# Kernel tuning notes

Measured on AMD Instinct MI355X. Metric: run time of the kernel, lower is better.

The kernel has to match this reference:

```python
import jax, jax.numpy as jnp
import numpy as np

EPS = 1e-6
BETA = 0.25
COMMIT_W = 1.0


def setup_inputs() -> dict:
    key = jax.random.key(0)
    k1, k2, k3 = jax.random.split(key, 3)
    b, c, h, w = 8, 256, 32, 32
    n_e, e_dim = 16384, 256
    z = jax.random.normal(k1, (b, c, h, w), jnp.float32)
    # frozen_codebook = randn(n_e, e_dim) * e_dim**-0.5
    codebook = jax.random.normal(k2, (n_e, e_dim), jnp.float32) * (e_dim ** -0.5)
    # nn.Linear(e_dim, in_channels, bias=False) weight: (in_channels, e_dim)
    W = jax.random.normal(k3, (c, e_dim), jnp.float32) * (e_dim ** -0.5)
    return {"z": z, "codebook": codebook, "W": W}


def _rotate_to(src, tgt):
    # Rotation trick (Fifty et al.): rotate src onto tgt direction with a
    # detached Householder-style transform; gradient flows through src only.
    # src, tgt: (n, d)
    norm_src = jnp.linalg.norm(src, axis=-1, keepdims=True)
    norm_tgt = jnp.linalg.norm(tgt, axis=-1, keepdims=True)
    u = src / (norm_src + EPS)
    q = tgt / (norm_tgt + EPS)
    uq = u + q
    w_ = jax.lax.stop_gradient(uq / (jnp.linalg.norm(uq, axis=-1, keepdims=True) + EPS))
    u_d = jax.lax.stop_gradient(u)
    q_d = jax.lax.stop_gradient(q)
    rot = (src
           - 2.0 * jnp.sum(src * w_, axis=-1, keepdims=True) * w_
           + 2.0 * jnp.sum(src * u_d, axis=-1, keepdims=True) * q_d)
    return rot * jax.lax.stop_gradient(norm_tgt / (norm_src + EPS))


def reference(z, codebook, W):
    b, c, h, w = z.shape
    # b c h w -> (b*h*w, c)
    z_flat = jnp.transpose(z, (0, 2, 3, 1)).reshape(-1, c)
    # implicit codebook: frozen codes through linear projection
    emb = codebook @ W.T  # (n_e, c)
    # squared L2 distances (no grad needed for argmin)
    d = (jnp.sum(z_flat ** 2, axis=1, keepdims=True)
         + jnp.sum(emb ** 2, axis=1)
         - 2.0 * (z_flat @ emb.T))  # (n_tok, n_e)
    indices = jnp.argmin(d, axis=1)  # (n_tok,)
    z_q_flat = emb[indices]  # gather quantized vectors
    loss = COMMIT_W * (jnp.mean((jax.lax.stop_gradient(z_flat) - z_q_flat) ** 2)
                       + BETA * jnp.mean((z_flat - jax.lax.stop_gradient(z_q_flat)) ** 2))
    z_q_flat = _rotate_to(z_flat, z_q_flat)
    z_q = jnp.transpose(z_q_flat.reshape(b, h, w, c), (0, 3, 1, 2))
    return z_q, loss, indices
```

## Files before the change

### kernel.cpp

```cpp
#include <hip/hip_runtime.h>
#include <math.h>

#define EPSV 1e-6f
#define NTOK 8192
#define NE   16384
#define DIM  256

using short8 = __attribute__((ext_vector_type(8))) short;
using f32x4v = __attribute__((ext_vector_type(4))) float;

__device__ __forceinline__ unsigned short f2bf(float v) {
    unsigned int u = __float_as_uint(v);
    u += 0x7fffu + ((u >> 16) & 1u);
    return (unsigned short)(u >> 16);
}
__device__ __forceinline__ float bf2f(unsigned short h) {
    return __uint_as_float(((unsigned int)h) << 16);
}

__device__ __forceinline__ void gload_lds16(const void* g, void* s) {
    __builtin_amdgcn_global_load_lds(
        (const __attribute__((address_space(1))) void*)g,
        (__attribute__((address_space(3))) void*)s, 16, 0, 0);
}

__device__ __forceinline__ void split8(const float4 a, const float4 b,
                                       short8& h, short8& l) {
    float f[8] = {a.x, a.y, a.z, a.w, b.x, b.y, b.z, b.w};
#pragma unroll
    for (int j = 0; j < 8; ++j) {
        unsigned short hh = f2bf(f[j]);
        h[j] = (short)hh;
        l[j] = (short)f2bf(f[j] - bf2f(hh));
    }
}

__global__ __launch_bounds__(256) void f1_pre(
    const float* __restrict__ zin, float* __restrict__ z_flat,
    unsigned short* __restrict__ zh, unsigned short* __restrict__ zl,
    float* __restrict__ sz, const float* __restrict__ Wm,
    unsigned short* __restrict__ wh, unsigned short* __restrict__ wl) {
    const int bid = blockIdx.x;
    const int tid = threadIdx.x;
    if (bid >= 128) {
        const int i = ((bid - 128) * 256 + tid) * 4;
        const float4 v = *(const float4*)(Wm + i);
        float f[4] = {v.x, v.y, v.z, v.w};
#pragma unroll
        for (int j = 0; j < 4; ++j) {
            unsigned short h = f2bf(f[j]);
            wh[i + j] = h;
            wl[i + j] = f2bf(f[j] - bf2f(h));
        }
        return;
    }
    __shared__ float tile[64][65];
    const int yx0 = (bid & 15) * 64, b = bid >> 4;
    const int sub = tid >> 6, ln = tid & 63;
    double dacc[16];
#pragma unroll
    for (int j = 0; j < 16; ++j) dacc[j] = 0.0;

    for (int cc = 0; cc < 4; ++cc) {
        const int c0 = cc * 64;
        __syncthreads();
#pragma unroll
        for (int j = 0; j < 16; ++j) {
            int cl = j * 4 + sub;
            tile[cl][ln] = zin[((size_t)(b * 256 + c0 + cl) << 10) + yx0 + ln];
        }
        __syncthreads();
#pragma unroll
        for (int j = 0; j < 16; ++j) {
            int tl = j * 4 + sub;
            float v = tile[ln][tl];
            size_t o = (size_t)(b * 1024 + yx0 + tl) * 256 + c0 + ln;
            z_flat[o] = v;
            unsigned short h = f2bf(v);
            zh[o] = h;
            zl[o] = f2bf(v - bf2f(h));
            dacc[j] += (double)v * v;
        }
    }
#pragma unroll
    for (int j = 0; j < 16; ++j) {
        double s = dacc[j];
#pragma unroll
        for (int m = 1; m < 64; m <<= 1) s += __shfl_xor(s, m);
        if (ln == 0) sz[b * 1024 + yx0 + j * 4 + sub] = (float)s;
    }
}

__global__ __launch_bounds__(256, 2) void k0c_emb(
    const float* __restrict__ cb, const unsigned short* __restrict__ wh,
    const unsigned short* __restrict__ wl, float* __restrict__ emb,
    unsigned short* __restrict__ eh, unsigned short* __restrict__ el,
    float* __restrict__ se0, float* __restrict__ se1) {
    __shared__ char smemC[65536];
    const int tid = threadIdx.x;
    const int w = tid >> 6, lane = tid & 63;
    const int quad = lane >> 4, lr = lane & 15;
    const int wr = w & 1, wc = w >> 1;
    const int n0 = blockIdx.x * 128, c0 = blockIdx.y * 128;

    f32x4v acc[4][4];
#pragma unroll
    for (int mt = 0; mt < 4; ++mt)
#pragma unroll
        for (int nt = 0; nt < 4; ++nt)
            acc[mt][nt] = (f32x4v){0.f, 0.f, 0.f, 0.f};

    for (int kc = 0; kc < 4; ++kc) {
        __syncthreads();
#pragma unroll
        for (int i = 0; i < 16; ++i) {
            int s = i * 4 + w;
            int u = s * 64 + lane;
            const void* g;
            if (s < 32) {
                int kg = u >> 7, row = u & 127;
                g = cb + (size_t)(n0 + row) * 256 + kc * 64 + kg * 4;
            } else if (s < 48) {
                int u1 = u - 2048;
                int kg = u1 >> 7, row = u1 & 127;
                g = wh + (size_t)(c0 + row) * 256 + kc * 64 + kg * 8;
            } else {
                int u2 = u - 3072;
                int kg = u2 >> 7, row = u2 & 127;
                g = wl + (size_t)(c0 + row) * 256 + kc * 64 + kg * 8;
            }
            gload_lds16(g, smemC + ((size_t)u << 4));
        }
        __syncthreads();
#pragma unroll
        for (int ks = 0; ks < 2; ++ks) {
            short8 Ah[4], Al[4], Bh[4], Bl[4];
#pragma unroll
            for (int mt = 0; mt < 4; ++mt) {
                int m = wr * 64 + mt * 16 + lr;
                int kg2 = ks * 8 + quad * 2;
                float4 f0 = *(const float4*)(smemC + (((size_t)kg2 * 128 + m) << 4));
                float4 f1 = *(const float4*)(smemC + ((((size_t)kg2 + 1) * 128 + m) << 4));
                split8(f0, f1, Ah[mt], Al[mt]);
            }
#pragma unroll
            for (int nt = 0; nt < 4; ++nt) {
                int n = wc * 64 + nt * 16 + lr;
                int ku = (ks * 4 + quad) * 128 + n;
                Bh[nt] = *(const short8*)(smemC + (((size_t)2048 + ku) << 4));
                Bl[nt] = *(const short8*)(smemC + (((size_t)3072 + ku) << 4));
            }
#pragma unroll
            for (int mt = 0; mt < 4; ++mt)
#pragma unroll
                for (int nt = 0; nt < 4; ++nt) {
                    f32x4v a = acc[mt][nt];
                    a = __builtin_amdgcn_mfma_f32_16x16x32_bf16(Ah[mt], Bh[nt], a, 0, 0, 0);
                    a = __builtin_amdgcn_mfma_f32_16x16x32_bf16(Ah[mt], Bl[nt], a, 0, 0, 0);
                    a = __builtin_amdgcn_mfma_f32_16x16x32_bf16(Al[mt], Bh[nt], a, 0, 0, 0);
                    a = __builtin_amdgcn_mfma_f32_16x16x32_bf16(Al[mt], Bl[nt], a, 0, 0, 0);
                    acc[mt][nt] = a;
                }
        }
    }
#pragma unroll
    for (int mt = 0; mt < 4; ++mt)
#pragma unroll
        for (int rr = 0; rr < 4; ++rr) {
            int row = n0 + wr * 64 + mt * 16 + quad * 4 + rr;
#pragma unroll
            for (int nt = 0; nt < 4; ++nt) {
                int col = c0 + wc * 64 + nt * 16 + lr;
                size_t o = (size_t)row * 256 + col;
                float v = acc[mt][nt][rr];
                emb[o] = v;
                unsigned short h = f2bf(v);
                eh[o] = h;
                el[o] = f2bf(v - bf2f(h));
            }
        }
    __syncthreads();
    float* sblk = (float*)smemC;
#pragma unroll
    for (int mt = 0; mt < 4; ++mt)
#pragma unroll
        for (int rr = 0; rr < 4; ++rr) {
            float s = 0.f;
#pragma unroll
            for (int nt = 0; nt < 4; ++nt) {
                float v = acc[mt][nt][rr];
                s = fmaf(v, v, s);
            }
#pragma unroll
            for (int st = 1; st < 16; st <<= 1) s += __shfl_xor(s, st);
            if (lr == 0)
                sblk[wc * 128 + wr * 64 + mt * 16 + quad * 4 + rr] = s;
        }
    __syncthreads();
    if (tid < 128) {
        float* sep = (blockIdx.y == 0) ? se0 : se1;
        sep[n0 + tid] = sblk[tid] + sblk[128 + tid];
    }
}

__global__ __launch_bounds__(256, 2) void k1_dist_argmin(
    const unsigned short* __restrict__ zh, const unsigned short* __restrict__ zl,
    const unsigned short* __restrict__ eh, const unsigned short* __restrict__ el,
    const float* __restrict__ sz, const float* __restrict__ se0,
    const float* __restrict__ se1, float* __restrict__ pval,
    int* __restrict__ pidx) {
    __shared__ short8 smem[2][2048];
    const int tid = threadIdx.x;
    const int w = tid >> 6, lane = tid & 63;
    const int quad = lane >> 4, lr = lane & 15;
    const int tokBase = blockIdx.x * 128;
    const int rowBase = tokBase + w * 32;
    const int slab = blockIdx.y;
    const int slabBase = slab * 2048;

    short8 Ah[2][8], Al[2][8];
#pragma unroll
    for (int mt = 0; mt < 2; ++mt)
#pragma unroll
        for (int ks = 0; ks < 8; ++ks) {
            size_t o = (size_t)(rowBase + mt * 16 + lr) * 256 + ks * 32 + quad * 8;
            Ah[mt][ks] = *(const short8*)(zh + o);
            Al[mt][ks] = *(const short8*)(zl + o);
        }

    float szr[2][4];
#pragma unroll
    for (int mt = 0; mt < 2; ++mt)
#pragma unroll
        for (int rr = 0; rr < 4; ++rr)
            szr[mt][rr] = sz[rowBase + mt * 16 + quad * 4 + rr];

    float minv[2][4];
    int mini[2][4];
#pragma unroll
    for (int mt = 0; mt < 2; ++mt)
#pragma unroll
        for (int rr = 0; rr < 4; ++rr) {
            minv[mt][rr] = INFINITY;
            mini[mt][rr] = 0;
        }

    auto stage = [&](int buf, int ch) {
        const int colBase = slabBase + ch * 32;
#pragma unroll
        for (int i = 0; i < 8; ++i) {
            int u = i * 256 + tid;
            int fmt = u >> 10;
            int u1 = u & 1023;
            int col = u1 >> 5, kgs = u1 & 31;
            int kg = kgs ^ col;
            const unsigned short* g =
                (fmt ? el : eh) + (size_t)(colBase + col) * 256 + kg * 8;
            gload_lds16(g, (char*)&smem[0][0] + buf * 32768 +
                               (((size_t)i * 256 + w * 64) << 4));
        }
    };

    stage(0, 0);
    __syncthreads();

    for (int ch = 0; ch < 64; ++ch) {
        const int cur = ch & 1;
        if (ch + 1 < 64) stage(cur ^ 1, ch + 1);

        const int colg0 = slabBase + ch * 32 + lr;
        const int colg1 = colg0 + 16;
        const float sec0 = se0[colg0] + se1[colg0];
        const float sec1 = se0[colg1] + se1[colg1];

        f32x4v acc[2][2];
#pragma unroll
        for (int mt = 0; mt < 2; ++mt)
#pragma unroll
            for (int nt = 0; nt < 2; ++nt)
                acc[mt][nt] = (f32x4v){0.f, 0.f, 0.f, 0.f};

#pragma unroll
        for (int ks = 0; ks < 8; ++ks) {
            short8 Bh[2], Bl[2];
#pragma unroll
            for (int nt = 0; nt < 2; ++nt) {
                int col = nt * 16 + lr;
                int kgs = (ks * 4 + quad) ^ col;
                Bh[nt] = smem[cur][col * 32 + kgs];
                Bl[nt] = smem[cur][1024 + col * 32 + kgs];
            }
#pragma unroll
            for (int mt = 0; mt < 2; ++mt)
#pragma unroll
                for (int nt = 0; nt < 2; ++nt) {
                    f32x4v a = acc[mt][nt];
                    a = __builtin_amdgcn_mfma_f32_16x16x32_bf16(Ah[mt][ks], Bh[nt], a, 0, 0, 0);
                    a = __builtin_amdgcn_mfma_f32_16x16x32_bf16(Ah[mt][ks], Bl[nt], a, 0, 0, 0);
                    a = __builtin_amdgcn_mfma_f32_16x16x32_bf16(Al[mt][ks], Bh[nt], a, 0, 0, 0);
                    acc[mt][nt] = a;
                }
        }

        const int colBase = slabBase + ch * 32;
#pragma unroll
        for (int nt = 0; nt < 2; ++nt) {
            const int colg = colBase + nt * 16 + lr;
            const float sec = nt ? sec1 : sec0;
#pragma unroll
            for (int mt = 0; mt < 2; ++mt)
#pragma unroll
                for (int rr = 0; rr < 4; ++rr) {
                    float szse = __fadd_rn(szr[mt][rr], sec);
                    float d = fmaf(-2.0f, acc[mt][nt][rr], szse);
                    if (d < minv[mt][rr]) {
                        minv[mt][rr] = d;
                        mini[mt][rr] = colg;
                    }
                }
        }
        __syncthreads();
    }

#pragma unroll
    for (int st = 1; st < 16; st <<= 1) {
#pragma unroll
        for (int mt = 0; mt < 2; ++mt)
#pragma unroll
            for (int rr = 0; rr < 4; ++rr) {
                float ov = __shfl_xor(minv[mt][rr], st);
                int oi = __shfl_xor(mini[mt][rr], st);
                if (ov < minv[mt][rr] ||
                    (ov == minv[mt][rr] && oi < mini[mt][rr])) {
                    minv[mt][rr] = ov;
                    mini[mt][rr] = oi;
                }
            }
    }
    if (lr == 0) {
#pragma unroll
        for (int mt = 0; mt < 2; ++mt)
#pragma unroll
            for (int rr = 0; rr < 4; ++rr) {
                int row = rowBase + mt * 16 + quad * 4 + rr;
                pval[(size_t)row * 8 + slab] = minv[mt][rr];
                pidx[(size_t)row * 8 + slab] = mini[mt][rr];
            }
    }
}

__global__ __launch_bounds__(256) void k3a_token(
    const float* __restrict__ z_flat, const float* __restrict__ emb,
    const float* __restrict__ pval, const int* __restrict__ pidx,
    float* __restrict__ alpha, float* __restrict__ beta,
    int* __restrict__ idxf, float* __restrict__ out,
    float* __restrict__ lpart) {
    __shared__ float red[4];
    const int w = threadIdx.x >> 6, lane = threadIdx.x & 63;
    const int t = blockIdx.x * 4 + w;

    float bv = INFINITY;
    int bi = 0x7fffffff;
    if (lane < 8) {
        bv = pval[(size_t)t * 8 + lane];
        bi = pidx[(size_t)t * 8 + lane];
    }
#pragma unroll
    for (int st = 1; st < 8; st <<= 1) {
        float ov = __shfl_xor(bv, st);
        int oi = __shfl_xor(bi, st);
        if (ov < bv || (ov == bv && oi < bi)) { bv = ov; bi = oi; }
    }
    const int best = __shfl(bi, 0);

    const float4 zv = *(const float4*)(z_flat + (size_t)t * 256 + lane * 4);
    const float4 ev = *(const float4*)(emb + (size_t)best * 256 + lane * 4);
    float szs = zv.x * zv.x + zv.y * zv.y + zv.z * zv.z + zv.w * zv.w;
    float ses = ev.x * ev.x + ev.y * ev.y + ev.z * ev.z + ev.w * ev.w;
    float zes = zv.x * ev.x + zv.y * ev.y + zv.z * ev.z + zv.w * ev.w;
    float dx = zv.x - ev.x, dy = zv.y - ev.y, dz = zv.z - ev.z, dw = zv.w - ev.w;
    float sqs = dx * dx + dy * dy + dz * dz + dw * dw;
#pragma unroll
    for (int m = 1; m < 64; m <<= 1) {
        szs += __shfl_xor(szs, m);
        ses += __shfl_xor(ses, m);
        zes += __shfl_xor(zes, m);
        sqs += __shfl_xor(sqs, m);
    }
    if (lane == 0) {
        float ns = sqrtf(szs), nt = sqrtf(ses);
        float inv_s = 1.0f / (ns + EPSV);
        float inv_t = 1.0f / (nt + EPSV);
        float s2 = szs * inv_s;
        float su = szs * inv_s * inv_s;
        float sq = ses * inv_t * inv_t;
        float uq = zes * inv_s * inv_t;
        float nw = sqrtf(su + sq + 2.0f * uq);
        float inv_w = 1.0f / (nw + EPSV);
        float s1 = (s2 + zes * inv_t) * inv_w;
        float scale = nt * inv_s;
        float a = scale * (1.0f - 2.0f * s1 * inv_w * inv_s);
        float bb = scale * inv_t * 2.0f * (s2 - s1 * inv_w);
        alpha[t] = a;
        beta[t] = bb;
        idxf[t] = best;
        out[2097153 + t] = (float)best;
        red[w] = sqs;
    }
    __syncthreads();
    if (threadIdx.x == 0)
        lpart[blockIdx.x] = red[0] + red[1] + red[2] + red[3];
}

__global__ __launch_bounds__(256) void k3b_zq(
    const float* __restrict__ zin, const float* __restrict__ emb,
    const float* __restrict__ alpha, const float* __restrict__ beta,
    const int* __restrict__ idxf, const float* __restrict__ lpart,
    float* __restrict__ out) {
    if (blockIdx.x == 0) {
        __shared__ float red[4];
        const int tid = threadIdx.x;
        float s = 0.0f;
        for (int i = tid; i < 2048; i += 256) s += lpart[i];
#pragma unroll
        for (int m = 1; m < 64; m <<= 1) s += __shfl_xor(s, m);
        if ((tid & 63) == 0) red[tid >> 6] = s;
        __syncthreads();
        if (tid == 0)
            out[2097152] = 1.25f * (red[0] + red[1] + red[2] + red[3]) *
                           (1.0f / 2097152.0f);
    }
    const int i = blockIdx.x * 256 + threadIdx.x;
    const int c = (i >> 10) & 255;
    const int t = ((i >> 18) << 10) | (i & 1023);
    out[i] = alpha[t] * zin[i] + beta[t] * emb[(size_t)idxf[t] * 256 + c];
}

extern "C" void kernel_launch(void* const* d_in, const int* in_sizes, int n_in,
                              void* d_out, int out_size, void* d_ws,
                              size_t ws_size, hipStream_t stream) {
    (void)in_sizes; (void)n_in; (void)out_size; (void)ws_size;
    const float* zin = (const float*)d_in[0];
    const float* cb  = (const float*)d_in[1];
    const float* Wm  = (const float*)d_in[2];
    float* out = (float*)d_out;
    char* ws = (char*)d_ws;

    float*          z_flat = (float*)(ws + 0);
    unsigned short* zh     = (unsigned short*)(ws + 8388608);
    unsigned short* zl     = (unsigned short*)(ws + 12582912);
    float*          emb    = (float*)(ws + 16777216);
    unsigned short* eh     = (unsigned short*)(ws + 33554432);
    unsigned short* el     = (unsigned short*)(ws + 41943040);
    float*          sz     = (float*)(ws + 50331648);
    float*          se0    = (float*)(ws + 50364416);
    float*          se1    = (float*)(ws + 50429952);
    float*          pval   = (float*)(ws + 50495488);
    int*            pidx   = (int*)(ws + 50757632);
    float*          alpha  = (float*)(ws + 51019776);
    float*          beta   = (float*)(ws + 51052544);
    int*            idxf   = (int*)(ws + 51085312);
    float*          lpart  = (float*)(ws + 51118080);
    unsigned short* wh     = (unsigned short*)(ws + 51126272);
    unsigned short* wl     = (unsigned short*)(ws + 51257344);

    f1_pre<<<192, 256, 0, stream>>>(zin, z_flat, zh, zl, sz, Wm, wh, wl);
    k0c_emb<<<dim3(128, 2), 256, 0, stream>>>(cb, wh, wl, emb, eh, el,
                                              se0, se1);
    k1_dist_argmin<<<dim3(64, 8), 256, 0, stream>>>(zh, zl, eh, el, sz,
                                                    se0, se1, pval, pidx);
    k3a_token<<<2048, 256, 0, stream>>>(z_flat, emb, pval, pidx, alpha, beta,
                                        idxf, out, lpart);
    k3b_zq<<<8192, 256, 0, stream>>>(zin, emb, alpha, beta, idxf, lpart, out);
}
```

Before: 286.7 us.

## Fuse preprocessing kernels, split W in-kernel, drop LDS swizzle, tile z_q transpose

The z transpose/split kernel and the codebook projection GEMM are merged into one launch, and W is split into hi/lo bf16 inside the GEMM, which removes the separate W conversion pass. The distance kernel's B-tile LDS layout changes from an XOR-swizzled layout to a linear one. k3a reuses the precomputed norms instead of recomputing them with reductions. k3b becomes a tiled kernel that reads z_flat and emb coalesced and transposes through LDS. The linear LDS layout may bring bank conflicts, and the extra split work now runs in every GEMM block.

After: 287.2 us. Within noise of the previous version (+0.2%).

```diff
diff --git a/kernel.cpp b/kernel.cpp
--- a/kernel.cpp
+++ b/kernel.cpp
@@ -35,73 +35,61 @@
     }
 }
 
-__global__ __launch_bounds__(256) void f1_pre(
+__global__ __launch_bounds__(256, 2) void f0_pre(
     const float* __restrict__ zin, float* __restrict__ z_flat,
     unsigned short* __restrict__ zh, unsigned short* __restrict__ zl,
-    float* __restrict__ sz, const float* __restrict__ Wm,
-    unsigned short* __restrict__ wh, unsigned short* __restrict__ wl) {
-    const int bid = blockIdx.x;
-    const int tid = threadIdx.x;
-    if (bid >= 128) {
-        const int i = ((bid - 128) * 256 + tid) * 4;
-        const float4 v = *(const float4*)(Wm + i);
-        float f[4] = {v.x, v.y, v.z, v.w};
-#pragma unroll
-        for (int j = 0; j < 4; ++j) {
-            unsigned short h = f2bf(f[j]);
-            wh[i + j] = h;
-            wl[i + j] = f2bf(f[j] - bf2f(h));
-        }
-        return;
-    }
-    __shared__ float tile[64][65];
-    const int yx0 = (bid & 15) * 64, b = bid >> 4;
-    const int sub = tid >> 6, ln = tid & 63;
-    double dacc[16];
-#pragma unroll
-    for (int j = 0; j < 16; ++j) dacc[j] = 0.0;
-
-    for (int cc = 0; cc < 4; ++cc) {
-        const int c0 = cc * 64;
-        __syncthreads();
-#pragma unroll
-        for (int j = 0; j < 16; ++j) {
-            int cl = j * 4 + sub;
-            tile[cl][ln] = zin[((size_t)(b * 256 + c0 + cl) << 10) + yx0 + ln];
-        }
-        __syncthreads();
-#pragma unroll
-        for (int j = 0; j < 16; ++j) {
-            int tl = j * 4 + sub;
-            float v = tile[ln][tl];
-            size_t o = (size_t)(b * 1024 + yx0 + tl) * 256 + c0 + ln;
-            z_flat[o] = v;
-            unsigned short h = f2bf(v);
-            zh[o] = h;
-            zl[o] = f2bf(v - bf2f(h));
-            dacc[j] += (double)v * v;
-        }
-    }
-#pragma unroll
-    for (int j = 0; j < 16; ++j) {
-        double s = dacc[j];
-#pragma unroll
-        for (int m = 1; m < 64; m <<= 1) s += __shfl_xor(s, m);
-        if (ln == 0) sz[b * 1024 + yx0 + j * 4 + sub] = (float)s;
-    }
-}
-
-__global__ __launch_bounds__(256, 2) void k0c_emb(
-    const float* __restrict__ cb, const unsigned short* __restrict__ wh,
-    const unsigned short* __restrict__ wl, float* __restrict__ emb,
+    float* __restrict__ sz, const float* __restrict__ cb,
+    const float* __restrict__ Wm, float* __restrict__ emb,
     unsigned short* __restrict__ eh, unsigned short* __restrict__ el,
     float* __restrict__ se0, float* __restrict__ se1) {
     __shared__ char smemC[65536];
     const int tid = threadIdx.x;
+
+    if (blockIdx.x < 128) {
+        float (*tile)[65] = (float(*)[65])smemC;
+        const int bid = blockIdx.x;
+        const int yx0 = (bid & 15) * 64, b = bid >> 4;
+        const int sub = tid >> 6, ln = tid & 63;
+        double dacc[16];
+#pragma unroll
+        for (int j = 0; j < 16; ++j) dacc[j] = 0.0;
+
+        for (int cc = 0; cc < 4; ++cc) {
+            const int c0 = cc * 64;
+            __syncthreads();
+#pragma unroll
+            for (int j = 0; j < 16; ++j) {
+                int cl = j * 4 + sub;
+                tile[cl][ln] = zin[((size_t)(b * 256 + c0 + cl) << 10) + yx0 + ln];
+            }
+            __syncthreads();
+#pragma unroll
+            for (int j = 0; j < 16; ++j) {
+                int tl = j * 4 + sub;
+                float v = tile[ln][tl];
+                size_t o = (size_t)(b * 1024 + yx0 + tl) * 256 + c0 + ln;
+                z_flat[o] = v;
+                unsigned short h = f2bf(v);
+                zh[o] = h;
+                zl[o] = f2bf(v - bf2f(h));
+                dacc[j] += (double)v * v;
+            }
+        }
+#pragma unroll
+        for (int j = 0; j < 16; ++j) {
+            double s = dacc[j];
+#pragma unroll
+            for (int m = 1; m < 64; m <<= 1) s += __shfl_xor(s, m);
+            if (ln == 0) sz[b * 1024 + yx0 + j * 4 + sub] = (float)s;
+        }
+        return;
+    }
+
+    const int bid2 = blockIdx.x - 128;
     const int w = tid >> 6, lane = tid & 63;
     const int quad = lane >> 4, lr = lane & 15;
     const int wr = w & 1, wc = w >> 1;
-    const int n0 = blockIdx.x * 128, c0 = blockIdx.y * 128;
+    const int n0 = (bid2 & 127) * 128, c0 = (bid2 >> 7) * 128;
 
     f32x4v acc[4][4];
 #pragma unroll
@@ -120,14 +108,10 @@
             if (s < 32) {
                 int kg = u >> 7, row = u & 127;
                 g = cb + (size_t)(n0 + row) * 256 + kc * 64 + kg * 4;
-            } else if (s < 48) {
+            } else {
                 int u1 = u - 2048;
                 int kg = u1 >> 7, row = u1 & 127;
-                g = wh + (size_t)(c0 + row) * 256 + kc * 64 + kg * 8;
-            } else {
-                int u2 = u - 3072;
-                int kg = u2 >> 7, row = u2 & 127;
-                g = wl + (size_t)(c0 + row) * 256 + kc * 64 + kg * 8;
+                g = Wm + (size_t)(c0 + row) * 256 + kc * 64 + kg * 4;
             }
             gload_lds16(g, smemC + ((size_t)u << 4));
         }
@@ -146,9 +130,10 @@
 #pragma unroll
             for (int nt = 0; nt < 4; ++nt) {
                 int n = wc * 64 + nt * 16 + lr;
-                int ku = (ks * 4 + quad) * 128 + n;
-                Bh[nt] = *(const short8*)(smemC + (((size_t)2048 + ku) << 4));
-                Bl[nt] = *(const short8*)(smemC + (((size_t)3072 + ku) << 4));
+                int kg2 = ks * 8 + quad * 2;
+                float4 g0 = *(const float4*)(smemC + (((size_t)(2048 + kg2 * 128 + n)) << 4));
+                float4 g1 = *(const float4*)(smemC + (((size_t)(2048 + (kg2 + 1) * 128 + n)) << 4));
+                split8(g0, g1, Bh[nt], Bl[nt]);
             }
 #pragma unroll
             for (int mt = 0; mt < 4; ++mt)
@@ -198,7 +183,7 @@
         }
     __syncthreads();
     if (tid < 128) {
-        float* sep = (blockIdx.y == 0) ? se0 : se1;
+        float* sep = ((bid2 >> 7) == 0) ? se0 : se1;
         sep[n0 + tid] = sblk[tid] + sblk[128 + tid];
     }
 }
@@ -209,7 +194,7 @@
     const float* __restrict__ sz, const float* __restrict__ se0,
     const float* __restrict__ se1, float* __restrict__ pval,
     int* __restrict__ pidx) {
-    __shared__ short8 smem[2][2048];
+    __shared__ char smem[65536];
     const int tid = threadIdx.x;
     const int w = tid >> 6, lane = tid & 63;
     const int quad = lane >> 4, lr = lane & 15;
@@ -252,17 +237,17 @@
             int u = i * 256 + tid;
             int fmt = u >> 10;
             int u1 = u & 1023;
-            int col = u1 >> 5, kgs = u1 & 31;
-            int kg = kgs ^ col;
+            int kg = u1 >> 5, col = u1 & 31;
             const unsigned short* g =
                 (fmt ? el : eh) + (size_t)(colBase + col) * 256 + kg * 8;
-            gload_lds16(g, (char*)&smem[0][0] + buf * 32768 +
-                               (((size_t)i * 256 + w * 64) << 4));
+            gload_lds16(g, smem + buf * 32768 + ((size_t)u << 4));
         }
     };
 
     stage(0, 0);
     __syncthreads();
+
+    const int bOff = quad * 512 + lr * 16;
 
     for (int ch = 0; ch < 64; ++ch) {
         const int cur = ch & 1;
@@ -280,15 +265,14 @@
             for (int nt = 0; nt < 2; ++nt)
                 acc[mt][nt] = (f32x4v){0.f, 0.f, 0.f, 0.f};
 
+        const char* p0 = smem + cur * 32768 + bOff;
 #pragma unroll
         for (int ks = 0; ks < 8; ++ks) {
             short8 Bh[2], Bl[2];
 #pragma unroll
             for (int nt = 0; nt < 2; ++nt) {
-                int col = nt * 16 + lr;
-                int kgs = (ks * 4 + quad) ^ col;
-                Bh[nt] = smem[cur][col * 32 + kgs];
-                Bl[nt] = smem[cur][1024 + col * 32 + kgs];
+                Bh[nt] = *(const short8*)(p0 + (ks * 2048 + nt * 256));
+                Bl[nt] = *(const short8*)(p0 + (16384 + ks * 2048 + nt * 256));
             }
 #pragma unroll
             for (int mt = 0; mt < 2; ++mt)
@@ -352,9 +336,10 @@
 __global__ __launch_bounds__(256) void k3a_token(
     const float* __restrict__ z_flat, const float* __restrict__ emb,
     const float* __restrict__ pval, const int* __restrict__ pidx,
-    float* __restrict__ alpha, float* __restrict__ beta,
-    int* __restrict__ idxf, float* __restrict__ out,
-    float* __restrict__ lpart) {
+    const float* __restrict__ sz, const float* __restrict__ se0,
+    const float* __restrict__ se1, float* __restrict__ alpha,
+    float* __restrict__ beta, int* __restrict__ idxf,
+    float* __restrict__ out, float* __restrict__ lpart) {
     __shared__ float red[4];
     const int w = threadIdx.x >> 6, lane = threadIdx.x & 63;
     const int t = blockIdx.x * 4 + w;
@@ -375,19 +360,14 @@
 
     const float4 zv = *(const float4*)(z_flat + (size_t)t * 256 + lane * 4);
     const float4 ev = *(const float4*)(emb + (size_t)best * 256 + lane * 4);
-    float szs = zv.x * zv.x + zv.y * zv.y + zv.z * zv.z + zv.w * zv.w;
-    float ses = ev.x * ev.x + ev.y * ev.y + ev.z * ev.z + ev.w * ev.w;
     float zes = zv.x * ev.x + zv.y * ev.y + zv.z * ev.z + zv.w * ev.w;
-    float dx = zv.x - ev.x, dy = zv.y - ev.y, dz = zv.z - ev.z, dw = zv.w - ev.w;
-    float sqs = dx * dx + dy * dy + dz * dz + dw * dw;
-#pragma unroll
-    for (int m = 1; m < 64; m <<= 1) {
-        szs += __shfl_xor(szs, m);
-        ses += __shfl_xor(ses, m);
-        zes += __shfl_xor(zes, m);
-        sqs += __shfl_xor(sqs, m);
-    }
+#pragma unroll
+    for (int m = 1; m < 64; m <<= 1) zes += __shfl_xor(zes, m);
+
     if (lane == 0) {
+        const float szs = sz[t];
+        const float ses = se0[best] + se1[best];
+        const float sqs = szs + ses - 2.0f * zes;
         float ns = sqrtf(szs), nt = sqrtf(ses);
         float inv_s = 1.0f / (ns + EPSV);
         float inv_t = 1.0f / (nt + EPSV);
@@ -413,13 +393,19 @@
 }
 
 __global__ __launch_bounds__(256) void k3b_zq(
-    const float* __restrict__ zin, const float* __restrict__ emb,
+    const float* __restrict__ z_flat, const float* __restrict__ emb,
     const float* __restrict__ alpha, const float* __restrict__ beta,
     const int* __restrict__ idxf, const float* __restrict__ lpart,
     float* __restrict__ out) {
-    if (blockIdx.x == 0) {
+    __shared__ float Q[64][65];
+    __shared__ float Asm[64], Bsm[64];
+    __shared__ int Ism[64];
+    const int tid = threadIdx.x;
+    const int t0 = blockIdx.x * 64;
+    const int c0 = blockIdx.y * 64;
+
+    if (blockIdx.x == 0 && blockIdx.y == 0) {
         __shared__ float red[4];
-        const int tid = threadIdx.x;
         float s = 0.0f;
         for (int i = tid; i < 2048; i += 256) s += lpart[i];
 #pragma unroll
@@ -430,10 +416,29 @@
             out[2097152] = 1.25f * (red[0] + red[1] + red[2] + red[3]) *
                            (1.0f / 2097152.0f);
     }
-    const int i = blockIdx.x * 256 + threadIdx.x;
-    const int c = (i >> 10) & 255;
-    const int t = ((i >> 18) << 10) | (i & 1023);
-    out[i] = alpha[t] * zin[i] + beta[t] * emb[(size_t)idxf[t] * 256 + c];
+
+    if (tid < 64) {
+        Asm[tid] = alpha[t0 + tid];
+        Bsm[tid] = beta[t0 + tid];
+        Ism[tid] = idxf[t0 + tid];
+    }
+    __syncthreads();
+
+    const int sub = tid >> 6, ln = tid & 63;
+#pragma unroll
+    for (int j = 0; j < 16; ++j) {
+        int tl = j * 4 + sub;
+        float e = emb[(size_t)Ism[tl] * 256 + c0 + ln];
+        float zv = z_flat[(size_t)(t0 + tl) * 256 + c0 + ln];
+        Q[tl][ln] = Asm[tl] * zv + Bsm[tl] * e;
+    }
+    __syncthreads();
+    const int b = t0 >> 10, yx0 = t0 & 1023;
+#pragma unroll
+    for (int j = 0; j < 16; ++j) {
+        int cl = j * 4 + sub;
+        out[((size_t)(b * 256 + c0 + cl) << 10) + yx0 + ln] = Q[ln][cl];
+    }
 }
 
 extern "C" void kernel_launch(void* const* d_in, const int* in_sizes, int n_in,
@@ -461,15 +466,13 @@
     float*          beta   = (float*)(ws + 51052544);
     int*            idxf   = (int*)(ws + 51085312);
     float*          lpart  = (float*)(ws + 51118080);
-    unsigned short* wh     = (unsigned short*)(ws + 51126272);
-    unsigned short* wl     = (unsigned short*)(ws + 51257344);
-
-    f1_pre<<<192, 256, 0, stream>>>(zin, z_flat, zh, zl, sz, Wm, wh, wl);
-    k0c_emb<<<dim3(128, 2), 256, 0, stream>>>(cb, wh, wl, emb, eh, el,
-                                              se0, se1);
+
+    f0_pre<<<384, 256, 0, stream>>>(zin, z_flat, zh, zl, sz, cb, Wm,
+                                    emb, eh, el, se0, se1);
     k1_dist_argmin<<<dim3(64, 8), 256, 0, stream>>>(zh, zl, eh, el, sz,
                                                     se0, se1, pval, pidx);
-    k3a_token<<<2048, 256, 0, stream>>>(z_flat, emb, pval, pidx, alpha, beta,
-                                        idxf, out, lpart);
-    k3b_zq<<<8192, 256, 0, stream>>>(zin, emb, alpha, beta, idxf, lpart, out);
-}
+    k3a_token<<<2048, 256, 0, stream>>>(z_flat, emb, pval, pidx, sz, se0, se1,
+                                        alpha, beta, idxf, out, lpart);
+    k3b_zq<<<dim3(128, 4), 256, 0, stream>>>(z_flat, emb, alpha, beta, idxf,
+                                             lpart, out);
+}
```
